# Performance work log

Measured on AMD Instinct MI355X. Metric: run time of the kernel, lower is better.

## Reference

```python
import jax, jax.numpy as jnp
import numpy as np

WINDOW_SIZE = 64  # matches init_kwargs


def _local_allowed_mask(L, window_size):
    # Original torch code: for query i, keys in slice [max(i-w//2,0) : min(i+w//2, L)) are allowed.
    half = window_size // 2
    i = jnp.arange(L)[:, None]
    j = jnp.arange(L)[None, :]
    return (j >= i - half) & (j < i + half)  # [L, L] bool, True = attend


def setup_inputs() -> dict:
    key = jax.random.key(0)
    kq, kk, kv = jax.random.split(key, 3)
    B, L, H, E, D = 4, 2048, 16, 64, 64
    queries = jax.random.normal(kq, (B, L, H, E), dtype=jnp.float32)
    keys = jax.random.normal(kk, (B, L, H, E), dtype=jnp.float32)
    values = jax.random.normal(kv, (B, L, H, D), dtype=jnp.float32)
    attn_mask = jnp.zeros((1,), dtype=bool)  # unused by the module
    return {"queries": queries, "keys": keys, "values": values, "attn_mask": attn_mask}


def reference(queries, keys, values, attn_mask):
    B, L, H, E = queries.shape
    scale = 1.0 / np.sqrt(E).astype(np.float32)
    allowed = _local_allowed_mask(L, WINDOW_SIZE)  # [L, L]
    # Dense scores, as in the original module (einsum 'blhe,bshe->bhls')
    scores = jnp.einsum('blhe,bshe->bhls', queries, keys)
    neg_inf = jnp.asarray(-jnp.inf, dtype=scores.dtype)
    scores = jnp.where(allowed[None, None, :, :], scores, neg_inf)
    A = jax.nn.softmax(scale * scores, axis=-1)  # [B, H, L, S]
    V = jnp.einsum('bhls,bshd->blhd', A, values)  # [B, L, H, D]
    return V
```

## Files before the change

kernel.cpp:

```cpp
#include <hip/hip_runtime.h>


#define B_ 4
#define L_ 2048
#define H_ 16
#define E_ 64
#define D_ 64
#define KS_STRIDE 72
#define VT_STRIDE 152
#define P_STRIDE 104

typedef __attribute__((ext_vector_type(8))) short short8;
typedef __attribute__((ext_vector_type(4))) float f32x4;

__device__ __forceinline__ unsigned int f2bf(float x) {
  unsigned int b = __float_as_uint(x);
  b += 0x7fffu + ((b >> 16) & 1u);
  return b >> 16;
}
__device__ __forceinline__ unsigned int pack2(float a, float b) {
  return f2bf(a) | (f2bf(b) << 16);
}
__device__ __forceinline__ short8 pack8(const f32x4& a, const f32x4& b) {
  union { short8 s; uint4 u; } r;
  r.u = make_uint4(pack2(a[0], a[1]), pack2(a[2], a[3]),
                   pack2(b[0], b[1]), pack2(b[2], b[3]));
  return r.s;
}
__device__ __forceinline__ int clampL(int k) {
  return k < 0 ? 0 : (k > (L_ - 1) ? (L_ - 1) : k);
}

__global__ __launch_bounds__(256, 4)
void local_attn_mfma(const float* __restrict__ qg,
                     const float* __restrict__ kg,
                     const float* __restrict__ vg,
                     float* __restrict__ og) {
  __shared__ __align__(16) unsigned short Ks[128 * KS_STRIDE];
  __shared__ __align__(16) unsigned short Vt[64 * VT_STRIDE];

  const int t = threadIdx.x;
  const int q0 = blockIdx.x * 64;
  const int h = blockIdx.y;
  const int b = blockIdx.z;
  const int kstart = q0 - 32;
  const int wave = t >> 6;
  const int lane = t & 63;
  const int col16 = lane & 15;
  const int quad = lane >> 4;

  f32x4 kf[8];
  #pragma unroll
  for (int it = 0; it < 8; ++it) {
    int cid = t + it * 256;
    int row = cid >> 4, ch = cid & 15;
    int key = clampL(kstart + row);
    kf[it] = *(const f32x4*)(kg + ((size_t)(b * L_ + key) * H_ + h) * E_ + ch * 4);
  }
  const int kp = t >> 2;
  const int dq = t & 3;
  f32x4 va[4], vc[4];
  {
    int k0 = clampL(kstart + 2 * kp);
    int k1 = clampL(kstart + 2 * kp + 1);
    const float* p0 = vg + ((size_t)(b * L_ + k0) * H_ + h) * D_ + dq * 16;
    const float* p1 = vg + ((size_t)(b * L_ + k1) * H_ + h) * D_ + dq * 16;
    #pragma unroll
    for (int i = 0; i < 4; ++i) va[i] = *(const f32x4*)(p0 + i * 4);
    #pragma unroll
    for (int i = 0; i < 4; ++i) vc[i] = *(const f32x4*)(p1 + i * 4);
  }

  asm volatile("" ::
      "v"(kf[0]), "v"(kf[1]), "v"(kf[2]), "v"(kf[3]),
      "v"(kf[4]), "v"(kf[5]), "v"(kf[6]), "v"(kf[7]),
      "v"(va[0]), "v"(va[1]), "v"(va[2]), "v"(va[3]),
      "v"(vc[0]), "v"(vc[1]), "v"(vc[2]), "v"(vc[3]));
  __builtin_amdgcn_sched_barrier(0);

  f32x4 qf0, qf1, qf2, qf3;
  {
    const float* p = qg + ((size_t)(b * L_ + q0 + wave * 16 + col16) * H_ + h) * E_ + quad * 8;
    qf0 = *(const f32x4*)p;
    qf1 = *(const f32x4*)(p + 4);
    qf2 = *(const f32x4*)(p + 32);
    qf3 = *(const f32x4*)(p + 36);
  }

  #pragma unroll
  for (int it = 0; it < 8; ++it) {
    int cid = t + it * 256;
    int row = cid >> 4, ch = cid & 15;
    f32x4 f = kf[it];
    *(uint2*)&Ks[row * KS_STRIDE + ch * 4] =
        make_uint2(pack2(f[0], f[1]), pack2(f[2], f[3]));
  }
  #pragma unroll
  for (int i = 0; i < 4; ++i) {
    #pragma unroll
    for (int j = 0; j < 4; ++j) {
      int d = dq * 16 + i * 4 + j;
      *(unsigned int*)&Vt[d * VT_STRIDE + 2 * kp] = pack2(va[i][j], vc[i][j]);
    }
  }
  *(uint2*)&Vt[(t >> 2) * VT_STRIDE + 128 + (t & 3) * 4] = make_uint2(0u, 0u);

  const short8 qa0 = pack8(qf0, qf1);
  const short8 qa1 = pack8(qf2, qf3);
  __syncthreads();

  f32x4 acc[5];
  #pragma unroll
  for (int tt = 0; tt < 5; ++tt) {
    int krow = wave * 16 + tt * 16 + col16;
    short8 b0 = *(const short8*)&Ks[krow * KS_STRIDE + quad * 8];
    short8 b1 = *(const short8*)&Ks[krow * KS_STRIDE + quad * 8 + 32];
    f32x4 c = {0.f, 0.f, 0.f, 0.f};
    c = __builtin_amdgcn_mfma_f32_16x16x32_bf16(qa0, b0, c, 0, 0, 0);
    c = __builtin_amdgcn_mfma_f32_16x16x32_bf16(qa1, b1, c, 0, 0, 0);
    acc[tt] = c;
  }

  #pragma unroll
  for (int r = 0; r < 4; ++r) {
    const int row_loc = quad * 4 + r;
    float x[5];
    #pragma unroll
    for (int tt = 0; tt < 5; ++tt) {
      int c_loc = tt * 16 + col16;
      int gkey = kstart + wave * 16 + c_loc;
      bool ok = (c_loc >= row_loc) && (c_loc < row_loc + 64) && (gkey >= 0) && (gkey < L_);
      x[tt] = ok ? acc[tt][r] * 0.125f : -1e30f;
    }
    float m = fmaxf(fmaxf(fmaxf(x[0], x[1]), fmaxf(x[2], x[3])), x[4]);
    m = fmaxf(m, __shfl_xor(m, 1));
    m = fmaxf(m, __shfl_xor(m, 2));
    m = fmaxf(m, __shfl_xor(m, 4));
    m = fmaxf(m, __shfl_xor(m, 8));
    float s = 0.f;
    #pragma unroll
    for (int tt = 0; tt < 5; ++tt) { x[tt] = __expf(x[tt] - m); s += x[tt]; }
    s += __shfl_xor(s, 1);
    s += __shfl_xor(s, 2);
    s += __shfl_xor(s, 4);
    s += __shfl_xor(s, 8);
    float inv = 1.0f / s;
    #pragma unroll
    for (int tt = 0; tt < 5; ++tt) acc[tt][r] = x[tt] * inv;
  }

  __syncthreads();

  unsigned short* Pw = &Ks[wave * 16 * P_STRIDE];
  *(uint2*)&Pw[col16 * P_STRIDE + 80 + quad * 4] = make_uint2(0u, 0u);
  #pragma unroll
  for (int tt = 0; tt < 5; ++tt)
    #pragma unroll
    for (int r = 0; r < 4; ++r)
      Pw[(quad * 4 + r) * P_STRIDE + tt * 16 + col16] = (unsigned short)f2bf(acc[tt][r]);

  f32x4 oacc[4];
  #pragma unroll
  for (int nt = 0; nt < 4; ++nt) oacc[nt] = (f32x4){0.f, 0.f, 0.f, 0.f};
  #pragma unroll
  for (int ks = 0; ks < 3; ++ks) {
    short8 pa = *(const short8*)&Pw[col16 * P_STRIDE + ks * 32 + quad * 8];
    #pragma unroll
    for (int nt = 0; nt < 4; ++nt) {
      short8 vb = *(const short8*)&Vt[(nt * 16 + col16) * VT_STRIDE + wave * 16 + ks * 32 + quad * 8];
      oacc[nt] = __builtin_amdgcn_mfma_f32_16x16x32_bf16(pa, vb, oacc[nt], 0, 0, 0);
    }
  }

  #pragma unroll
  for (int r = 0; r < 4; ++r) {
    int q = q0 + wave * 16 + quad * 4 + r;
    float* orow = og + ((size_t)(b * L_ + q) * H_ + h) * D_;
    #pragma unroll
    for (int nt = 0; nt < 4; ++nt)
      orow[nt * 16 + col16] = oacc[nt][r];
  }
}

extern "C" void kernel_launch(void* const* d_in, const int* in_sizes, int n_in,
                              void* d_out, int out_size, void* d_ws, size_t ws_size,
                              hipStream_t stream) {
  const float* q = (const float*)d_in[0];
  const float* k = (const float*)d_in[1];
  const float* v = (const float*)d_in[2];
  float* o = (float*)d_out;
  dim3 grid(L_ / 64, H_, B_);
  local_attn_mfma<<<grid, dim3(256), 0, stream>>>(q, k, v, o);
}
```

Baseline: 138.2 us.

## Process four query tiles per block with double-buffered register prefetch

```diff
diff --git a/kernel.cpp b/kernel.cpp
--- a/kernel.cpp
+++ b/kernel.cpp
@@ -6,9 +6,12 @@
 #define H_ 16
 #define E_ 64
 #define D_ 64
+#define ST 4
 #define KS_STRIDE 72
 #define VT_STRIDE 152
 #define P_STRIDE 104
+#define KS_SZ (128 * KS_STRIDE)
+#define VT_SZ (64 * VT_STRIDE)
 
 typedef __attribute__((ext_vector_type(8))) short short8;
 typedef __attribute__((ext_vector_type(4))) float f32x4;
@@ -31,154 +34,197 @@
   return k < 0 ? 0 : (k > (L_ - 1) ? (L_ - 1) : k);
 }
 
-__global__ __launch_bounds__(256, 4)
-void local_attn_mfma(const float* __restrict__ qg,
-                     const float* __restrict__ kg,
-                     const float* __restrict__ vg,
-                     float* __restrict__ og) {
-  __shared__ __align__(16) unsigned short Ks[128 * KS_STRIDE];
-  __shared__ __align__(16) unsigned short Vt[64 * VT_STRIDE];
-
-  const int t = threadIdx.x;
-  const int q0 = blockIdx.x * 64;
-  const int h = blockIdx.y;
-  const int b = blockIdx.z;
+struct Pref {
+  f32x4 kf[8];
+  f32x4 va[4], vc[4];
+  f32x4 qf[4];
+};
+
+__device__ __forceinline__ void issue_loads(Pref& p,
+    const float* __restrict__ qg, const float* __restrict__ kg,
+    const float* __restrict__ vg, int b, int h, int q0,
+    int t, int wave, int col16, int quad) {
   const int kstart = q0 - 32;
-  const int wave = t >> 6;
-  const int lane = t & 63;
-  const int col16 = lane & 15;
-  const int quad = lane >> 4;
-
-  f32x4 kf[8];
   #pragma unroll
   for (int it = 0; it < 8; ++it) {
     int cid = t + it * 256;
     int row = cid >> 4, ch = cid & 15;
     int key = clampL(kstart + row);
-    kf[it] = *(const f32x4*)(kg + ((size_t)(b * L_ + key) * H_ + h) * E_ + ch * 4);
+    p.kf[it] = *(const f32x4*)(kg + ((size_t)(b * L_ + key) * H_ + h) * E_ + ch * 4);
   }
   const int kp = t >> 2;
   const int dq = t & 3;
-  f32x4 va[4], vc[4];
   {
     int k0 = clampL(kstart + 2 * kp);
     int k1 = clampL(kstart + 2 * kp + 1);
     const float* p0 = vg + ((size_t)(b * L_ + k0) * H_ + h) * D_ + dq * 16;
     const float* p1 = vg + ((size_t)(b * L_ + k1) * H_ + h) * D_ + dq * 16;
     #pragma unroll
-    for (int i = 0; i < 4; ++i) va[i] = *(const f32x4*)(p0 + i * 4);
-    #pragma unroll
-    for (int i = 0; i < 4; ++i) vc[i] = *(const f32x4*)(p1 + i * 4);
-  }
-
+    for (int i = 0; i < 4; ++i) p.va[i] = *(const f32x4*)(p0 + i * 4);
+    #pragma unroll
+    for (int i = 0; i < 4; ++i) p.vc[i] = *(const f32x4*)(p1 + i * 4);
+  }
+  {
+    const float* pq = qg + ((size_t)(b * L_ + q0 + wave * 16 + col16) * H_ + h) * E_ + quad * 8;
+    p.qf[0] = *(const f32x4*)pq;
+    p.qf[1] = *(const f32x4*)(pq + 4);
+    p.qf[2] = *(const f32x4*)(pq + 32);
+    p.qf[3] = *(const f32x4*)(pq + 36);
+  }
+}
+
+__device__ __forceinline__ void anchor(Pref& p) {
   asm volatile("" ::
-      "v"(kf[0]), "v"(kf[1]), "v"(kf[2]), "v"(kf[3]),
-      "v"(kf[4]), "v"(kf[5]), "v"(kf[6]), "v"(kf[7]),
-      "v"(va[0]), "v"(va[1]), "v"(va[2]), "v"(va[3]),
-      "v"(vc[0]), "v"(vc[1]), "v"(vc[2]), "v"(vc[3]));
+      "v"(p.kf[0]), "v"(p.kf[1]), "v"(p.kf[2]), "v"(p.kf[3]),
+      "v"(p.kf[4]), "v"(p.kf[5]), "v"(p.kf[6]), "v"(p.kf[7]),
+      "v"(p.va[0]), "v"(p.va[1]), "v"(p.va[2]), "v"(p.va[3]),
+      "v"(p.vc[0]), "v"(p.vc[1]), "v"(p.vc[2]), "v"(p.vc[3]),
+      "v"(p.qf[0]), "v"(p.qf[1]), "v"(p.qf[2]), "v"(p.qf[3]));
   __builtin_amdgcn_sched_barrier(0);
-
-  f32x4 qf0, qf1, qf2, qf3;
-  {
-    const float* p = qg + ((size_t)(b * L_ + q0 + wave * 16 + col16) * H_ + h) * E_ + quad * 8;
-    qf0 = *(const f32x4*)p;
-    qf1 = *(const f32x4*)(p + 4);
-    qf2 = *(const f32x4*)(p + 32);
-    qf3 = *(const f32x4*)(p + 36);
-  }
-
+}
+
+__device__ __forceinline__ void pack_stage(const Pref& p,
+    unsigned short* KsB, unsigned short* VtB,
+    short8& qa0, short8& qa1, int t) {
   #pragma unroll
   for (int it = 0; it < 8; ++it) {
     int cid = t + it * 256;
     int row = cid >> 4, ch = cid & 15;
-    f32x4 f = kf[it];
-    *(uint2*)&Ks[row * KS_STRIDE + ch * 4] =
+    f32x4 f = p.kf[it];
+    *(uint2*)&KsB[row * KS_STRIDE + ch * 4] =
         make_uint2(pack2(f[0], f[1]), pack2(f[2], f[3]));
   }
+  const int kp = t >> 2;
+  const int dq = t & 3;
   #pragma unroll
   for (int i = 0; i < 4; ++i) {
     #pragma unroll
     for (int j = 0; j < 4; ++j) {
       int d = dq * 16 + i * 4 + j;
-      *(unsigned int*)&Vt[d * VT_STRIDE + 2 * kp] = pack2(va[i][j], vc[i][j]);
-    }
-  }
-  *(uint2*)&Vt[(t >> 2) * VT_STRIDE + 128 + (t & 3) * 4] = make_uint2(0u, 0u);
-
-  const short8 qa0 = pack8(qf0, qf1);
-  const short8 qa1 = pack8(qf2, qf3);
+      *(unsigned int*)&VtB[d * VT_STRIDE + 2 * kp] = pack2(p.va[i][j], p.vc[i][j]);
+    }
+  }
+  qa0 = pack8(p.qf[0], p.qf[1]);
+  qa1 = pack8(p.qf[2], p.qf[3]);
+}
+
+__global__ __launch_bounds__(256, 2)
+void local_attn_mfma(const float* __restrict__ qg,
+                     const float* __restrict__ kg,
+                     const float* __restrict__ vg,
+                     float* __restrict__ og) {
+  __shared__ __align__(16) unsigned short Ks[2][KS_SZ];
+  __shared__ __align__(16) unsigned short Vt[2][VT_SZ];
+
+  const int t = threadIdx.x;
+  const int tile0 = blockIdx.x * ST;
+  const int h = blockIdx.y;
+  const int b = blockIdx.z;
+  const int wave = t >> 6;
+  const int lane = t & 63;
+  const int col16 = lane & 15;
+  const int quad = lane >> 4;
+
+  Pref pf;
+  issue_loads(pf, qg, kg, vg, b, h, tile0 * 64, t, wave, col16, quad);
+  short8 qa0, qa1;
+  pack_stage(pf, &Ks[0][0], &Vt[0][0], qa0, qa1, t);
+  *(uint2*)&Vt[0][(t >> 2) * VT_STRIDE + 128 + (t & 3) * 4] = make_uint2(0u, 0u);
+  *(uint2*)&Vt[1][(t >> 2) * VT_STRIDE + 128 + (t & 3) * 4] = make_uint2(0u, 0u);
   __syncthreads();
 
-  f32x4 acc[5];
-  #pragma unroll
-  for (int tt = 0; tt < 5; ++tt) {
-    int krow = wave * 16 + tt * 16 + col16;
-    short8 b0 = *(const short8*)&Ks[krow * KS_STRIDE + quad * 8];
-    short8 b1 = *(const short8*)&Ks[krow * KS_STRIDE + quad * 8 + 32];
-    f32x4 c = {0.f, 0.f, 0.f, 0.f};
-    c = __builtin_amdgcn_mfma_f32_16x16x32_bf16(qa0, b0, c, 0, 0, 0);
-    c = __builtin_amdgcn_mfma_f32_16x16x32_bf16(qa1, b1, c, 0, 0, 0);
-    acc[tt] = c;
-  }
-
-  #pragma unroll
-  for (int r = 0; r < 4; ++r) {
-    const int row_loc = quad * 4 + r;
-    float x[5];
+  #pragma unroll
+  for (int s = 0; s < ST; ++s) {
+    unsigned short* KsC = &Ks[s & 1][0];
+    unsigned short* VtC = &Vt[s & 1][0];
+    unsigned short* KsN = &Ks[(s + 1) & 1][0];
+    unsigned short* VtN = &Vt[(s + 1) & 1][0];
+    const int q0 = (tile0 + s) * 64;
+    const int kstart = q0 - 32;
+
+    if (s + 1 < ST) {
+      issue_loads(pf, qg, kg, vg, b, h, q0 + 64, t, wave, col16, quad);
+      anchor(pf);
+    }
+
+    f32x4 acc[5];
     #pragma unroll
     for (int tt = 0; tt < 5; ++tt) {
-      int c_loc = tt * 16 + col16;
-      int gkey = kstart + wave * 16 + c_loc;
-      bool ok = (c_loc >= row_loc) && (c_loc < row_loc + 64) && (gkey >= 0) && (gkey < L_);
-      x[tt] = ok ? acc[tt][r] * 0.125f : -1e30f;
-    }
-    float m = fmaxf(fmaxf(fmaxf(x[0], x[1]), fmaxf(x[2], x[3])), x[4]);
-    m = fmaxf(m, __shfl_xor(m, 1));
-    m = fmaxf(m, __shfl_xor(m, 2));
-    m = fmaxf(m, __shfl_xor(m, 4));
-    m = fmaxf(m, __shfl_xor(m, 8));
-    float s = 0.f;
-    #pragma unroll
-    for (int tt = 0; tt < 5; ++tt) { x[tt] = __expf(x[tt] - m); s += x[tt]; }
-    s += __shfl_xor(s, 1);
-    s += __shfl_xor(s, 2);
-    s += __shfl_xor(s, 4);
-    s += __shfl_xor(s, 8);
-    float inv = 1.0f / s;
-    #pragma unroll
-    for (int tt = 0; tt < 5; ++tt) acc[tt][r] = x[tt] * inv;
-  }
-
-  __syncthreads();
-
-  unsigned short* Pw = &Ks[wave * 16 * P_STRIDE];
-  *(uint2*)&Pw[col16 * P_STRIDE + 80 + quad * 4] = make_uint2(0u, 0u);
-  #pragma unroll
-  for (int tt = 0; tt < 5; ++tt)
-    #pragma unroll
-    for (int r = 0; r < 4; ++r)
-      Pw[(quad * 4 + r) * P_STRIDE + tt * 16 + col16] = (unsigned short)f2bf(acc[tt][r]);
-
-  f32x4 oacc[4];
-  #pragma unroll
-  for (int nt = 0; nt < 4; ++nt) oacc[nt] = (f32x4){0.f, 0.f, 0.f, 0.f};
-  #pragma unroll
-  for (int ks = 0; ks < 3; ++ks) {
-    short8 pa = *(const short8*)&Pw[col16 * P_STRIDE + ks * 32 + quad * 8];
-    #pragma unroll
-    for (int nt = 0; nt < 4; ++nt) {
-      short8 vb = *(const short8*)&Vt[(nt * 16 + col16) * VT_STRIDE + wave * 16 + ks * 32 + quad * 8];
-      oacc[nt] = __builtin_amdgcn_mfma_f32_16x16x32_bf16(pa, vb, oacc[nt], 0, 0, 0);
-    }
-  }
-
-  #pragma unroll
-  for (int r = 0; r < 4; ++r) {
-    int q = q0 + wave * 16 + quad * 4 + r;
-    float* orow = og + ((size_t)(b * L_ + q) * H_ + h) * D_;
-    #pragma unroll
-    for (int nt = 0; nt < 4; ++nt)
-      orow[nt * 16 + col16] = oacc[nt][r];
+      int krow = wave * 16 + tt * 16 + col16;
+      short8 b0 = *(const short8*)&KsC[krow * KS_STRIDE + quad * 8];
+      short8 b1 = *(const short8*)&KsC[krow * KS_STRIDE + quad * 8 + 32];
+      f32x4 c = {0.f, 0.f, 0.f, 0.f};
+      c = __builtin_amdgcn_mfma_f32_16x16x32_bf16(qa0, b0, c, 0, 0, 0);
+      c = __builtin_amdgcn_mfma_f32_16x16x32_bf16(qa1, b1, c, 0, 0, 0);
+      acc[tt] = c;
+    }
+
+    #pragma unroll
+    for (int r = 0; r < 4; ++r) {
+      const int row_loc = quad * 4 + r;
+      float x[5];
+      #pragma unroll
+      for (int tt = 0; tt < 5; ++tt) {
+        int c_loc = tt * 16 + col16;
+        int gkey = kstart + wave * 16 + c_loc;
+        bool ok = (c_loc >= row_loc) && (c_loc < row_loc + 64) && (gkey >= 0) && (gkey < L_);
+        x[tt] = ok ? acc[tt][r] * 0.125f : -1e30f;
+      }
+      float m = fmaxf(fmaxf(fmaxf(x[0], x[1]), fmaxf(x[2], x[3])), x[4]);
+      m = fmaxf(m, __shfl_xor(m, 1));
+      m = fmaxf(m, __shfl_xor(m, 2));
+      m = fmaxf(m, __shfl_xor(m, 4));
+      m = fmaxf(m, __shfl_xor(m, 8));
+      float sum = 0.f;
+      #pragma unroll
+      for (int tt = 0; tt < 5; ++tt) { x[tt] = __expf(x[tt] - m); sum += x[tt]; }
+      sum += __shfl_xor(sum, 1);
+      sum += __shfl_xor(sum, 2);
+      sum += __shfl_xor(sum, 4);
+      sum += __shfl_xor(sum, 8);
+      float inv = 1.0f / sum;
+      #pragma unroll
+      for (int tt = 0; tt < 5; ++tt) acc[tt][r] = x[tt] * inv;
+    }
+
+    __syncthreads();
+
+    unsigned short* Pw = &KsC[wave * 16 * P_STRIDE];
+    *(uint2*)&Pw[col16 * P_STRIDE + 80 + quad * 4] = make_uint2(0u, 0u);
+    #pragma unroll
+    for (int tt = 0; tt < 5; ++tt)
+      #pragma unroll
+      for (int r = 0; r < 4; ++r)
+        Pw[(quad * 4 + r) * P_STRIDE + tt * 16 + col16] = (unsigned short)f2bf(acc[tt][r]);
+
+    short8 qn0, qn1;
+    if (s + 1 < ST) pack_stage(pf, KsN, VtN, qn0, qn1, t);
+
+    __syncthreads();
+
+    f32x4 oacc[4];
+    #pragma unroll
+    for (int nt = 0; nt < 4; ++nt) oacc[nt] = (f32x4){0.f, 0.f, 0.f, 0.f};
+    #pragma unroll
+    for (int ks = 0; ks < 3; ++ks) {
+      short8 pa = *(const short8*)&Pw[col16 * P_STRIDE + ks * 32 + quad * 8];
+      #pragma unroll
+      for (int nt = 0; nt < 4; ++nt) {
+        short8 vb = *(const short8*)&VtC[(nt * 16 + col16) * VT_STRIDE + wave * 16 + ks * 32 + quad * 8];
+        oacc[nt] = __builtin_amdgcn_mfma_f32_16x16x32_bf16(pa, vb, oacc[nt], 0, 0, 0);
+      }
+    }
+
+    #pragma unroll
+    for (int r = 0; r < 4; ++r) {
+      int q = q0 + wave * 16 + quad * 4 + r;
+      float* orow = og + ((size_t)(b * L_ + q) * H_ + h) * D_;
+      #pragma unroll
+      for (int nt = 0; nt < 4; ++nt)
+        orow[nt * 16 + col16] = oacc[nt][r];
+    }
+
+    if (s + 1 < ST) { qa0 = qn0; qa1 = qn1; }
   }
 }
 
@@ -189,6 +235,6 @@
   const float* k = (const float*)d_in[1];
   const float* v = (const float*)d_in[2];
   float* o = (float*)d_out;
-  dim3 grid(L_ / 64, H_, B_);
+  dim3 grid(L_ / (64 * ST), H_, B_);
   local_attn_mfma<<<grid, dim3(256), 0, stream>>>(q, k, v, o);
 }
```

Result: slower. 146.4 us (+6.0%).

## Compute transposed scores so softmax and P stay in registers

Applied to the files above, without the earlier changes.

```diff
diff --git a/kernel.cpp b/kernel.cpp
--- a/kernel.cpp
+++ b/kernel.cpp
@@ -6,9 +6,7 @@
 #define H_ 16
 #define E_ 64
 #define D_ 64
-#define KS_STRIDE 72
 #define VT_STRIDE 152
-#define P_STRIDE 104
 
 typedef __attribute__((ext_vector_type(8))) short short8;
 typedef __attribute__((ext_vector_type(4))) float f32x4;
@@ -31,12 +29,11 @@
   return k < 0 ? 0 : (k > (L_ - 1) ? (L_ - 1) : k);
 }
 
-__global__ __launch_bounds__(256, 4)
+__global__ __launch_bounds__(256, 8)
 void local_attn_mfma(const float* __restrict__ qg,
                      const float* __restrict__ kg,
                      const float* __restrict__ vg,
                      float* __restrict__ og) {
-  __shared__ __align__(16) unsigned short Ks[128 * KS_STRIDE];
   __shared__ __align__(16) unsigned short Vt[64 * VT_STRIDE];
 
   const int t = threadIdx.x;
@@ -49,20 +46,12 @@
   const int col16 = lane & 15;
   const int quad = lane >> 4;
 
-  f32x4 kf[8];
-  #pragma unroll
-  for (int it = 0; it < 8; ++it) {
-    int cid = t + it * 256;
-    int row = cid >> 4, ch = cid & 15;
-    int key = clampL(kstart + row);
-    kf[it] = *(const f32x4*)(kg + ((size_t)(b * L_ + key) * H_ + h) * E_ + ch * 4);
-  }
   const int kp = t >> 2;
   const int dq = t & 3;
   f32x4 va[4], vc[4];
   {
-    int k0 = clampL(kstart + 2 * kp);
-    int k1 = clampL(kstart + 2 * kp + 1);
+    const int k0 = clampL(kstart + 2 * kp);
+    const int k1 = clampL(kstart + 2 * kp + 1);
     const float* p0 = vg + ((size_t)(b * L_ + k0) * H_ + h) * D_ + dq * 16;
     const float* p1 = vg + ((size_t)(b * L_ + k1) * H_ + h) * D_ + dq * 16;
     #pragma unroll
@@ -71,110 +60,109 @@
     for (int i = 0; i < 4; ++i) vc[i] = *(const f32x4*)(p1 + i * 4);
   }
 
-  asm volatile("" ::
-      "v"(kf[0]), "v"(kf[1]), "v"(kf[2]), "v"(kf[3]),
-      "v"(kf[4]), "v"(kf[5]), "v"(kf[6]), "v"(kf[7]),
-      "v"(va[0]), "v"(va[1]), "v"(va[2]), "v"(va[3]),
-      "v"(vc[0]), "v"(vc[1]), "v"(vc[2]), "v"(vc[3]));
-  __builtin_amdgcn_sched_barrier(0);
-
-  f32x4 qf0, qf1, qf2, qf3;
+  short8 qa0, qa1;
   {
-    const float* p = qg + ((size_t)(b * L_ + q0 + wave * 16 + col16) * H_ + h) * E_ + quad * 8;
-    qf0 = *(const f32x4*)p;
-    qf1 = *(const f32x4*)(p + 4);
-    qf2 = *(const f32x4*)(p + 32);
-    qf3 = *(const f32x4*)(p + 36);
+    const float* pq = qg + ((size_t)(b * L_ + q0 + wave * 16 + col16) * H_ + h) * E_ + quad * 8;
+    f32x4 qf0 = *(const f32x4*)pq;
+    f32x4 qf1 = *(const f32x4*)(pq + 4);
+    f32x4 qf2 = *(const f32x4*)(pq + 32);
+    f32x4 qf3 = *(const f32x4*)(pq + 36);
+    qa0 = pack8(qf0, qf1);
+    qa1 = pack8(qf2, qf3);
   }
 
   #pragma unroll
-  for (int it = 0; it < 8; ++it) {
-    int cid = t + it * 256;
-    int row = cid >> 4, ch = cid & 15;
-    f32x4 f = kf[it];
-    *(uint2*)&Ks[row * KS_STRIDE + ch * 4] =
-        make_uint2(pack2(f[0], f[1]), pack2(f[2], f[3]));
-  }
-  #pragma unroll
-  for (int i = 0; i < 4; ++i) {
+  for (int i = 0; i < 4; ++i)
     #pragma unroll
     for (int j = 0; j < 4; ++j) {
       int d = dq * 16 + i * 4 + j;
       *(unsigned int*)&Vt[d * VT_STRIDE + 2 * kp] = pack2(va[i][j], vc[i][j]);
     }
-  }
   *(uint2*)&Vt[(t >> 2) * VT_STRIDE + 128 + (t & 3) * 4] = make_uint2(0u, 0u);
 
-  const short8 qa0 = pack8(qf0, qf1);
-  const short8 qa1 = pack8(qf2, qf3);
   __syncthreads();
 
   f32x4 acc[5];
   #pragma unroll
   for (int tt = 0; tt < 5; ++tt) {
-    int krow = wave * 16 + tt * 16 + col16;
-    short8 b0 = *(const short8*)&Ks[krow * KS_STRIDE + quad * 8];
-    short8 b1 = *(const short8*)&Ks[krow * KS_STRIDE + quad * 8 + 32];
+    const int key = clampL(kstart + wave * 16 + tt * 16 + col16);
+    const float* pk = kg + ((size_t)(b * L_ + key) * H_ + h) * E_ + quad * 8;
+    f32x4 k0 = *(const f32x4*)pk;
+    f32x4 k1 = *(const f32x4*)(pk + 4);
+    f32x4 k2 = *(const f32x4*)(pk + 32);
+    f32x4 k3 = *(const f32x4*)(pk + 36);
+    short8 kb0 = pack8(k0, k1);
+    short8 kb1 = pack8(k2, k3);
     f32x4 c = {0.f, 0.f, 0.f, 0.f};
-    c = __builtin_amdgcn_mfma_f32_16x16x32_bf16(qa0, b0, c, 0, 0, 0);
-    c = __builtin_amdgcn_mfma_f32_16x16x32_bf16(qa1, b1, c, 0, 0, 0);
+    c = __builtin_amdgcn_mfma_f32_16x16x32_bf16(kb0, qa0, c, 0, 0, 0);
+    c = __builtin_amdgcn_mfma_f32_16x16x32_bf16(kb1, qa1, c, 0, 0, 0);
     acc[tt] = c;
   }
 
-  #pragma unroll
-  for (int r = 0; r < 4; ++r) {
-    const int row_loc = quad * 4 + r;
-    float x[5];
-    #pragma unroll
-    for (int tt = 0; tt < 5; ++tt) {
-      int c_loc = tt * 16 + col16;
-      int gkey = kstart + wave * 16 + c_loc;
-      bool ok = (c_loc >= row_loc) && (c_loc < row_loc + 64) && (gkey >= 0) && (gkey < L_);
-      x[tt] = ok ? acc[tt][r] * 0.125f : -1e30f;
-    }
-    float m = fmaxf(fmaxf(fmaxf(x[0], x[1]), fmaxf(x[2], x[3])), x[4]);
-    m = fmaxf(m, __shfl_xor(m, 1));
-    m = fmaxf(m, __shfl_xor(m, 2));
-    m = fmaxf(m, __shfl_xor(m, 4));
-    m = fmaxf(m, __shfl_xor(m, 8));
-    float s = 0.f;
-    #pragma unroll
-    for (int tt = 0; tt < 5; ++tt) { x[tt] = __expf(x[tt] - m); s += x[tt]; }
-    s += __shfl_xor(s, 1);
-    s += __shfl_xor(s, 2);
-    s += __shfl_xor(s, 4);
-    s += __shfl_xor(s, 8);
-    float inv = 1.0f / s;
-    #pragma unroll
-    for (int tt = 0; tt < 5; ++tt) acc[tt][r] = x[tt] * inv;
-  }
-
-  __syncthreads();
-
-  unsigned short* Pw = &Ks[wave * 16 * P_STRIDE];
-  *(uint2*)&Pw[col16 * P_STRIDE + 80 + quad * 4] = make_uint2(0u, 0u);
+  float mx = -1e30f;
   #pragma unroll
   for (int tt = 0; tt < 5; ++tt)
     #pragma unroll
-    for (int r = 0; r < 4; ++r)
-      Pw[(quad * 4 + r) * P_STRIDE + tt * 16 + col16] = (unsigned short)f2bf(acc[tt][r]);
+    for (int r = 0; r < 4; ++r) {
+      const int k_loc = tt * 16 + quad * 4 + r;
+      const int gkey = kstart + wave * 16 + k_loc;
+      const bool ok = (k_loc >= col16) && (k_loc < col16 + 64) &&
+                      (gkey >= 0) && (gkey < L_);
+      const float v = ok ? acc[tt][r] * 0.125f : -1e30f;
+      acc[tt][r] = v;
+      mx = fmaxf(mx, v);
+    }
+  mx = fmaxf(mx, __shfl_xor(mx, 16));
+  mx = fmaxf(mx, __shfl_xor(mx, 32));
+  float s = 0.f;
+  #pragma unroll
+  for (int tt = 0; tt < 5; ++tt)
+    #pragma unroll
+    for (int r = 0; r < 4; ++r) {
+      const float e = __expf(acc[tt][r] - mx);
+      acc[tt][r] = e;
+      s += e;
+    }
+  s += __shfl_xor(s, 16);
+  s += __shfl_xor(s, 32);
+  const float inv = 1.0f / s;
+
+  short8 pa[3];
+  {
+    union { short8 s8; uint4 u4; } w;
+    w.u4 = make_uint4(pack2(acc[0][0] * inv, acc[0][1] * inv),
+                      pack2(acc[0][2] * inv, acc[0][3] * inv),
+                      pack2(acc[1][0] * inv, acc[1][1] * inv),
+                      pack2(acc[1][2] * inv, acc[1][3] * inv));
+    pa[0] = w.s8;
+    w.u4 = make_uint4(pack2(acc[2][0] * inv, acc[2][1] * inv),
+                      pack2(acc[2][2] * inv, acc[2][3] * inv),
+                      pack2(acc[3][0] * inv, acc[3][1] * inv),
+                      pack2(acc[3][2] * inv, acc[3][3] * inv));
+    pa[1] = w.s8;
+    w.u4 = make_uint4(pack2(acc[4][0] * inv, acc[4][1] * inv),
+                      pack2(acc[4][2] * inv, acc[4][3] * inv), 0u, 0u);
+    pa[2] = w.s8;
+  }
 
   f32x4 oacc[4];
   #pragma unroll
   for (int nt = 0; nt < 4; ++nt) oacc[nt] = (f32x4){0.f, 0.f, 0.f, 0.f};
   #pragma unroll
-  for (int ks = 0; ks < 3; ++ks) {
-    short8 pa = *(const short8*)&Pw[col16 * P_STRIDE + ks * 32 + quad * 8];
+  for (int nt = 0; nt < 4; ++nt) {
+    const int rowb = (nt * 16 + col16) * VT_STRIDE;
     #pragma unroll
-    for (int nt = 0; nt < 4; ++nt) {
-      short8 vb = *(const short8*)&Vt[(nt * 16 + col16) * VT_STRIDE + wave * 16 + ks * 32 + quad * 8];
-      oacc[nt] = __builtin_amdgcn_mfma_f32_16x16x32_bf16(pa, vb, oacc[nt], 0, 0, 0);
+    for (int ks = 0; ks < 3; ++ks) {
+      union { short8 s8; uint2 u2[2]; } vb;
+      vb.u2[0] = *(const uint2*)&Vt[rowb + wave * 16 + ks * 32 + quad * 4];
+      vb.u2[1] = *(const uint2*)&Vt[rowb + wave * 16 + ks * 32 + 16 + quad * 4];
+      oacc[nt] = __builtin_amdgcn_mfma_f32_16x16x32_bf16(pa[ks], vb.s8, oacc[nt], 0, 0, 0);
     }
   }
 
   #pragma unroll
   for (int r = 0; r < 4; ++r) {
-    int q = q0 + wave * 16 + quad * 4 + r;
+    const int q = q0 + wave * 16 + quad * 4 + r;
     float* orow = og + ((size_t)(b * L_ + q) * H_ + h) * D_;
     #pragma unroll
     for (int nt = 0; nt < 4; ++nt)
```

Result: slower. 152.6 us (+10.4%).
